# Optimization experiments

Measured on AMD Instinct MI355X. Metric: run time of the kernel, lower is better.

## Reference

```python
import jax, jax.numpy as jnp
import numpy as np

S = 2048      # words in the sentence
LMAX = 16     # max chars per word (padded)
VOCAB = 50000
ALPHA = 256
CE = 256      # char_embedding_dim (also char-LSTM hidden)
WE = 512      # word_embedding_dim
H = 1024      # hidden_dim of word LSTM


def setup_inputs() -> dict:
    key = jax.random.key(0)
    ks = jax.random.split(key, 13)
    def u(k, shape, scale):
        return jax.random.uniform(k, shape, jnp.float32, -scale, scale)
    sc_c = 1.0 / np.sqrt(CE).astype(np.float32)   # torch LSTM init scale
    sc_w = 1.0 / np.sqrt(H).astype(np.float32)
    return {
        "word_idxs": jax.random.randint(ks[0], (S,), 0, VOCAB),
        "char_idxs": jax.random.randint(ks[1], (S, LMAX), 0, ALPHA),
        "char_lens": jax.random.randint(ks[2], (S,), 1, LMAX + 1),
        "char_emb": jax.random.normal(ks[3], (ALPHA, CE), jnp.float32) * 0.1,
        "word_emb": jax.random.normal(ks[4], (VOCAB, WE), jnp.float32) * 0.1,
        "Wih_c": u(ks[5], (4 * CE, CE), sc_c),
        "Whh_c": u(ks[6], (4 * CE, CE), sc_c),
        "bih_c": u(ks[7], (4 * CE,), sc_c),
        "bhh_c": u(ks[8], (4 * CE,), sc_c),
        "Wih_w": u(ks[9], (4 * H, WE + CE), sc_w),
        "Whh_w": u(ks[10], (4 * H, H), sc_w),
        "bih_w": u(ks[11], (4 * H,), sc_w),
        "bhh_w": u(ks[12], (4 * H,), sc_w),
    }


def _lstm_scan(xs, Wih, Whh, bih, bhh, hdim):
    """Single-layer LSTM, torch gate order (i, f, g, o). xs: [T, B, D] -> hs [T, B, hdim]."""
    B = xs.shape[1]
    bias = bih + bhh
    def step(carry, x):
        h, c = carry
        gates = x @ Wih.T + h @ Whh.T + bias  # [B, 4*hdim]
        i, f, g, o = jnp.split(gates, 4, axis=-1)
        c = jax.nn.sigmoid(f) * c + jax.nn.sigmoid(i) * jnp.tanh(g)
        h = jax.nn.sigmoid(o) * jnp.tanh(c)
        return (h, c), h
    init = (jnp.zeros((B, hdim), xs.dtype), jnp.zeros((B, hdim), xs.dtype))
    _, hs = jax.lax.scan(step, init, xs)
    return hs


def reference(word_idxs, char_idxs, char_lens, char_emb, word_emb,
              Wih_c, Whh_c, bih_c, bhh_c, Wih_w, Whh_w, bih_w, bhh_w):
    # Char LSTM: batch all S words together (fuses the per-word Python loop).
    # Causality makes output at t = len-1 identical to running the true-length seq.
    ce = char_emb[char_idxs]                  # [S, LMAX, CE]
    ce = jnp.swapaxes(ce, 0, 1)               # [LMAX, S, CE] time-major
    hs = _lstm_scan(ce, Wih_c, Whh_c, bih_c, bhh_c, CE)   # [LMAX, S, CE]
    hs = jnp.swapaxes(hs, 0, 1)               # [S, LMAX, CE]
    last = jnp.take_along_axis(hs, (char_lens - 1)[:, None, None], axis=1)[:, 0]  # [S, CE]

    we = word_emb[word_idxs]                  # [S, WE]
    lstm_in = jnp.concatenate([we, last], axis=-1)[:, None, :]  # [S, 1, WE+CE]
    out = _lstm_scan(lstm_in, Wih_w, Whh_w, bih_w, bhh_w, H)    # [S, 1, H]
    # dropout p=0.0 -> identity
    return out
```

## Files before the change

### kernel.cpp

```cpp
#include <hip/hip_runtime.h>
#include <stdint.h>

#define S_WORDS 2048
#define LMAX    16
#define CE      256
#define WE      512
#define HDIM    1024
#define GC      1024
#define GW      4096
#define KW      768
#define NWG_RNN 128
#define NWB_WIN 512

#define IN_GATES_OFF 0
#define LAST_OFF     33554432
#define WT2C_OFF     35651584
#define WT2W_OFF     37748736
#define RING_OFF     WT2C_OFF
#define FLAGS_OFF    (RING_OFF + 3 * HDIM * 8)

typedef float f32x4 __attribute__((ext_vector_type(4)));

static __device__ __forceinline__ float sigm(float x) { return 1.0f / (1.0f + __expf(-x)); }
static __device__ __forceinline__ float tanh_fast(float x) {
    float ax = fminf(fabsf(x), 15.0f);
    float e  = __expf(2.0f * ax);
    float t  = (e - 1.0f) / (e + 1.0f);
    return copysignf(t, x);
}

__global__ void prep_c_kernel(const float* __restrict__ Wih,
                              const float* __restrict__ Whh,
                              float2* __restrict__ WT2c) {
    int idx = blockIdx.x * blockDim.x + threadIdx.x;
    if (idx >= 256 * GC) return;
    int kp = idx >> 10, row = idx & (GC - 1);
    int k = kp * 2;
    float2 v;
    if (k < CE) { v.x = Wih[row * CE + k];      v.y = Wih[row * CE + k + 1]; }
    else        { v.x = Whh[row * CE + k - CE]; v.y = Whh[row * CE + k - CE + 1]; }
    WT2c[idx] = v;
}

__global__ void prep_w_kernel(const float* __restrict__ Wih,
                              float2* __restrict__ WT2w) {
    int idx = blockIdx.x * blockDim.x + threadIdx.x;
    if (idx >= 384 * GW) return;
    int kp = idx >> 12, row = idx & (GW - 1);
    float2 v;
    v.x = Wih[row * KW + 2 * kp];
    v.y = Wih[row * KW + 2 * kp + 1];
    WT2w[idx] = v;
}

__global__ void __launch_bounds__(256) char_lstm_kernel(
    const int* __restrict__ char_idxs,
    const int* __restrict__ char_lens,
    const float* __restrict__ char_emb,
    const float* __restrict__ bih,
    const float* __restrict__ bhh,
    const float2* __restrict__ WT2c,
    float* __restrict__ last_out)
{
    __shared__ float xh[8][2 * CE];
    const int j = threadIdx.x;
    const int wbase = blockIdx.x * 8;

    float bias[4];
    #pragma unroll
    for (int g = 0; g < 4; g++) bias[g] = bih[g * CE + j] + bhh[g * CE + j];

    int len[8];
    float c[8];
    #pragma unroll
    for (int w = 0; w < 8; w++) {
        c[w] = 0.0f;
        xh[w][CE + j] = 0.0f;
        len[w] = char_lens[wbase + w];
    }

    for (int t = 0; t < LMAX; t++) {
        #pragma unroll
        for (int w = 0; w < 8; w++) {
            int ci = char_idxs[(wbase + w) * LMAX + t];
            xh[w][j] = char_emb[ci * CE + j];
        }
        __syncthreads();

        float acc[4][8];
        #pragma unroll
        for (int g = 0; g < 4; g++)
            #pragma unroll
            for (int w = 0; w < 8; w++) acc[g][w] = 0.0f;

        for (int kp = 0; kp < CE; kp++) {
            float2 wv[4];
            #pragma unroll
            for (int g = 0; g < 4; g++) wv[g] = WT2c[kp * GC + g * CE + j];
            #pragma unroll
            for (int w = 0; w < 8; w++) {
                float2 xv = *(const float2*)&xh[w][2 * kp];
                #pragma unroll
                for (int g = 0; g < 4; g++)
                    acc[g][w] = fmaf(wv[g].y, xv.y, fmaf(wv[g].x, xv.x, acc[g][w]));
            }
        }
        __syncthreads();

        #pragma unroll
        for (int w = 0; w < 8; w++) {
            float iv = sigm(acc[0][w] + bias[0]);
            float fv = sigm(acc[1][w] + bias[1]);
            float gv = tanhf(acc[2][w] + bias[2]);
            float ov = sigm(acc[3][w] + bias[3]);
            c[w] = fv * c[w] + iv * gv;
            float h = ov * tanhf(c[w]);
            xh[w][CE + j] = h;
            if (t == len[w] - 1) last_out[(wbase + w) * CE + j] = h;
        }
    }
}

__global__ void __launch_bounds__(512, 2) fused_word_kernel(
    const float* __restrict__ Whh,
    const int* __restrict__ word_idxs,
    const float* __restrict__ word_emb,
    const float* __restrict__ last,
    const float2* __restrict__ WT2w,
    const float* __restrict__ bih,
    const float* __restrict__ bhh,
    float* __restrict__ in_gates,
    unsigned long long* __restrict__ ring,
    unsigned int* __restrict__ flags,
    float* __restrict__ out)
{
    __shared__ float smem[8 * KW];
    const int tid = threadIdx.x;

    if (blockIdx.x >= NWG_RNN) {
        const int nb    = blockIdx.x - NWG_RNN;
        const int grp   = nb >> 1;
        const int half  = nb & 1;
        const int jj    = tid & 255;
        const int gh    = tid >> 8;
        const int rb2   = half * 2 + gh;
        const int wbase = grp * 8;
        float (*xh)[KW] = (float(*)[KW])smem;

        for (int w = 0; w < 8; w++) {
            int wi = word_idxs[wbase + w];
            xh[w][tid] = word_emb[(size_t)wi * WE + tid];
            if (tid < 256) xh[w][WE + tid] = last[(wbase + w) * CE + tid];
        }
        __syncthreads();

        float acc[4][8];
        #pragma unroll
        for (int g = 0; g < 4; g++)
            #pragma unroll
            for (int w = 0; w < 8; w++) acc[g][w] = 0.0f;

        for (int kp = 0; kp < KW / 2; kp++) {
            float2 wv[4];
            #pragma unroll
            for (int g = 0; g < 4; g++) wv[g] = WT2w[(size_t)kp * GW + rb2 * GC + g * CE + jj];
            #pragma unroll
            for (int w = 0; w < 8; w++) {
                float2 xv = *(const float2*)&xh[w][2 * kp];
                #pragma unroll
                for (int g = 0; g < 4; g++)
                    acc[g][w] = fmaf(wv[g].y, xv.y, fmaf(wv[g].x, xv.x, acc[g][w]));
            }
        }

        #pragma unroll
        for (int g = 0; g < 4; g++) {
            int row = rb2 * GC + g * CE + jj;
            float bias = bih[row] + bhh[row];
            #pragma unroll
            for (int w = 0; w < 8; w++)
                __hip_atomic_store(in_gates + (size_t)(wbase + w) * GW + row,
                                   acc[g][w] + bias,
                                   __ATOMIC_RELAXED, __HIP_MEMORY_SCOPE_AGENT);
        }
        __syncthreads();
        if (tid == 0)
            __hip_atomic_fetch_add(flags + grp, 1u,
                                   __ATOMIC_RELEASE, __HIP_MEMORY_SCOPE_AGENT);
        return;
    }

    const int v = tid >> 6;
    const int l = tid & 63;
    const int unit = blockIdx.x * 8 + v;
    float (*hbb)[HDIM] = (float(*)[HDIM])smem;

    f32x4 w[4][4];
    #pragma unroll
    for (int g = 0; g < 4; g++)
        #pragma unroll
        for (int cc = 0; cc < 4; cc++)
            w[g][cc] = *(const f32x4*)(Whh + (size_t)(g * HDIM + unit) * HDIM
                                       + cc * 256 + l * 4);
    #pragma unroll
    for (int g = 0; g < 4; g++)
        #pragma unroll
        for (int cc = 0; cc < 4; cc++)
            asm volatile("" : "+v"(w[g][cc]));

    float c_reg = 0.0f;

    for (int t = 0; t < S_WORDS; t++) {
        if ((t & 7) == 0) {
            const unsigned int* fl = flags + (t >> 3);
            while (__hip_atomic_load(fl, __ATOMIC_RELAXED, __HIP_MEMORY_SCOPE_AGENT) < 2u) {}
        }

        float ing0 = 0.f, ing1 = 0.f, ing2 = 0.f, ing3 = 0.f;
        if (l == 0) {
            const float* ig = in_gates + (size_t)t * GW + unit;
            ing0 = __hip_atomic_load(ig + 0 * HDIM, __ATOMIC_RELAXED, __HIP_MEMORY_SCOPE_AGENT);
            ing1 = __hip_atomic_load(ig + 1 * HDIM, __ATOMIC_RELAXED, __HIP_MEMORY_SCOPE_AGENT);
            ing2 = __hip_atomic_load(ig + 2 * HDIM, __ATOMIC_RELAXED, __HIP_MEMORY_SCOPE_AGENT);
            ing3 = __hip_atomic_load(ig + 3 * HDIM, __ATOMIC_RELAXED, __HIP_MEMORY_SCOPE_AGENT);
        }

        const unsigned long long* slot = ring + (size_t)(t % 3) * HDIM + v * 128;
        unsigned long long a0 = 0, a1 = 0;
        bool ok0 = false, ok1 = false;
        do {
            if (!ok0) {
                a0 = __hip_atomic_load(slot + l,      __ATOMIC_RELAXED, __HIP_MEMORY_SCOPE_AGENT);
                ok0 = ((unsigned)(a0 >> 32) == (unsigned)t);
            }
            if (!ok1) {
                a1 = __hip_atomic_load(slot + 64 + l, __ATOMIC_RELAXED, __HIP_MEMORY_SCOPE_AGENT);
                ok1 = ((unsigned)(a1 >> 32) == (unsigned)t);
            }
        } while (!__all(ok0 && ok1));
        {
            union { unsigned u32; float f; } c0, c1;
            c0.u32 = (unsigned)a0; c1.u32 = (unsigned)a1;
            hbb[t & 1][v * 128 + l]      = c0.f;
            hbb[t & 1][v * 128 + 64 + l] = c1.f;
        }
        __syncthreads();

        float acc0 = 0.f, acc1 = 0.f, acc2 = 0.f, acc3 = 0.f;
        const float* hb = hbb[t & 1];
        #pragma unroll
        for (int cc = 0; cc < 4; cc++) {
            f32x4 hv = *(const f32x4*)&hb[cc * 256 + l * 4];
            #pragma unroll
            for (int e = 0; e < 4; e++) {
                acc0 = fmaf(w[0][cc][e], hv[e], acc0);
                acc1 = fmaf(w[1][cc][e], hv[e], acc1);
                acc2 = fmaf(w[2][cc][e], hv[e], acc2);
                acc3 = fmaf(w[3][cc][e], hv[e], acc3);
            }
        }
        #pragma unroll
        for (int off = 32; off >= 1; off >>= 1) {
            acc0 += __shfl_xor(acc0, off, 64);
            acc1 += __shfl_xor(acc1, off, 64);
            acc2 += __shfl_xor(acc2, off, 64);
            acc3 += __shfl_xor(acc3, off, 64);
        }

        if (l == 0) {
            float iv = sigm(acc0 + ing0);
            float fv = sigm(acc1 + ing1);
            float gv = tanh_fast(acc2 + ing2);
            float ov = sigm(acc3 + ing3);
            c_reg = fv * c_reg + iv * gv;
            float h = ov * tanh_fast(c_reg);
            union { float f; unsigned u32; } cv; cv.f = h;
            unsigned long long pv =
                ((unsigned long long)(unsigned)(t + 1) << 32) | (unsigned long long)cv.u32;
            __hip_atomic_store(ring + (size_t)((t + 1) % 3) * HDIM + unit, pv,
                               __ATOMIC_RELAXED, __HIP_MEMORY_SCOPE_AGENT);
            out[(size_t)t * HDIM + unit] = h;
        }
    }
}

extern "C" void kernel_launch(void* const* d_in, const int* in_sizes, int n_in,
                              void* d_out, int out_size, void* d_ws, size_t ws_size,
                              hipStream_t stream) {
    const int* word_idxs = (const int*)d_in[0];
    const int* char_idxs = (const int*)d_in[1];
    const int* char_lens = (const int*)d_in[2];
    const float* char_emb = (const float*)d_in[3];
    const float* word_emb = (const float*)d_in[4];
    const float* Wih_c = (const float*)d_in[5];
    const float* Whh_c = (const float*)d_in[6];
    const float* bih_c = (const float*)d_in[7];
    const float* bhh_c = (const float*)d_in[8];
    const float* Wih_w = (const float*)d_in[9];
    const float* Whh_w = (const float*)d_in[10];
    const float* bih_w = (const float*)d_in[11];
    const float* bhh_w = (const float*)d_in[12];

    char* ws = (char*)d_ws;
    float*  in_gates = (float*)(ws + IN_GATES_OFF);
    float*  last     = (float*)(ws + LAST_OFF);
    float2* WT2c     = (float2*)(ws + WT2C_OFF);
    float2* WT2w     = (float2*)(ws + WT2W_OFF);
    unsigned long long* ring = (unsigned long long*)(ws + RING_OFF);
    unsigned int* flags      = (unsigned int*)(ws + FLAGS_OFF);

    hipLaunchKernelGGL(prep_c_kernel, dim3(1024), dim3(256), 0, stream,
                       Wih_c, Whh_c, WT2c);
    hipLaunchKernelGGL(prep_w_kernel, dim3(6144), dim3(256), 0, stream,
                       Wih_w, WT2w);
    hipLaunchKernelGGL(char_lstm_kernel, dim3(256), dim3(256), 0, stream,
                       char_idxs, char_lens, char_emb, bih_c, bhh_c, WT2c, last);
    hipMemsetAsync(ws + RING_OFF, 0,
                   3 * HDIM * sizeof(unsigned long long) + 256 * sizeof(unsigned int),
                   stream);
    hipLaunchKernelGGL(fused_word_kernel, dim3(NWG_RNN + NWB_WIN), dim3(512), 0, stream,
                       Whh_w, word_idxs, word_emb, last, WT2w, bih_w, bhh_w,
                       in_gates, ring, flags, (float*)d_out);
}
```

Before: 5.611 ms.

## Replace per-step workgroup barrier with per-wave LDS flags and chunked consumption

Removes the __syncthreads in the word-LSTM recurrence. Each wave publishes a workgroup-scope release flag once it has written its slice of h into LDS. Each wave then processes the four 256-element chunks in a staggered order, waiting only on the two waves that produced each chunk, so computation can start before every wave has arrived. The ring polling is double-buffered so two loads are in flight, and s_setprio raises wave priority during the critical compute phase. The risk is extra LDS flag traffic and spin overhead, and LDS size has to cover the flags.

```diff
diff --git a/kernel.cpp b/kernel.cpp
--- a/kernel.cpp
+++ b/kernel.cpp
@@ -20,6 +20,8 @@
 #define FLAGS_OFF    (RING_OFF + 3 * HDIM * 8)
 
 typedef float f32x4 __attribute__((ext_vector_type(4)));
+
+#define LD_AGENT(p) __hip_atomic_load((p), __ATOMIC_RELAXED, __HIP_MEMORY_SCOPE_AGENT)
 
 static __device__ __forceinline__ float sigm(float x) { return 1.0f / (1.0f + __expf(-x)); }
 static __device__ __forceinline__ float tanh_fast(float x) {
@@ -194,6 +196,9 @@
     const int l = tid & 63;
     const int unit = blockIdx.x * 8 + v;
     float (*hbb)[HDIM] = (float(*)[HDIM])smem;
+    unsigned int* hflag = (unsigned int*)(smem + 2 * HDIM);
+
+    if (tid < 8) hflag[tid] = 0u;
 
     f32x4 w[4][4];
     #pragma unroll
@@ -208,48 +213,77 @@
         for (int cc = 0; cc < 4; cc++)
             asm volatile("" : "+v"(w[g][cc]));
 
+    __syncthreads();
+
     float c_reg = 0.0f;
 
     for (int t = 0; t < S_WORDS; t++) {
         if ((t & 7) == 0) {
             const unsigned int* fl = flags + (t >> 3);
-            while (__hip_atomic_load(fl, __ATOMIC_RELAXED, __HIP_MEMORY_SCOPE_AGENT) < 2u) {}
+            while (LD_AGENT(fl) < 2u) {}
         }
 
         float ing0 = 0.f, ing1 = 0.f, ing2 = 0.f, ing3 = 0.f;
         if (l == 0) {
             const float* ig = in_gates + (size_t)t * GW + unit;
-            ing0 = __hip_atomic_load(ig + 0 * HDIM, __ATOMIC_RELAXED, __HIP_MEMORY_SCOPE_AGENT);
-            ing1 = __hip_atomic_load(ig + 1 * HDIM, __ATOMIC_RELAXED, __HIP_MEMORY_SCOPE_AGENT);
-            ing2 = __hip_atomic_load(ig + 2 * HDIM, __ATOMIC_RELAXED, __HIP_MEMORY_SCOPE_AGENT);
-            ing3 = __hip_atomic_load(ig + 3 * HDIM, __ATOMIC_RELAXED, __HIP_MEMORY_SCOPE_AGENT);
-        }
-
-        const unsigned long long* slot = ring + (size_t)(t % 3) * HDIM + v * 128;
-        unsigned long long a0 = 0, a1 = 0;
+            ing0 = LD_AGENT(ig + 0 * HDIM);
+            ing1 = LD_AGENT(ig + 1 * HDIM);
+            ing2 = LD_AGENT(ig + 2 * HDIM);
+            ing3 = LD_AGENT(ig + 3 * HDIM);
+        }
+
+        const unsigned long long* sA = ring + (size_t)(t % 3) * HDIM + v * 128 + l;
+        const unsigned long long* sB = sA + 64;
+        unsigned long long p0 = LD_AGENT(sA), p1 = LD_AGENT(sB);
+        unsigned long long q0 = LD_AGENT(sA), q1 = LD_AGENT(sB);
         bool ok0 = false, ok1 = false;
-        do {
-            if (!ok0) {
-                a0 = __hip_atomic_load(slot + l,      __ATOMIC_RELAXED, __HIP_MEMORY_SCOPE_AGENT);
-                ok0 = ((unsigned)(a0 >> 32) == (unsigned)t);
-            }
-            if (!ok1) {
-                a1 = __hip_atomic_load(slot + 64 + l, __ATOMIC_RELAXED, __HIP_MEMORY_SCOPE_AGENT);
-                ok1 = ((unsigned)(a1 >> 32) == (unsigned)t);
-            }
-        } while (!__all(ok0 && ok1));
+        unsigned long long h0 = 0, h1 = 0;
+        const unsigned tt = (unsigned)t;
+        for (;;) {
+            if (!ok0 && (unsigned)(p0 >> 32) == tt) { h0 = p0; ok0 = true; }
+            if (!ok1 && (unsigned)(p1 >> 32) == tt) { h1 = p1; ok1 = true; }
+            if (__all(ok0 && ok1)) break;
+            if (!ok0) p0 = LD_AGENT(sA);
+            if (!ok1) p1 = LD_AGENT(sB);
+            if (!ok0 && (unsigned)(q0 >> 32) == tt) { h0 = q0; ok0 = true; }
+            if (!ok1 && (unsigned)(q1 >> 32) == tt) { h1 = q1; ok1 = true; }
+            if (__all(ok0 && ok1)) break;
+            if (!ok0) q0 = LD_AGENT(sA);
+            if (!ok1) q1 = LD_AGENT(sB);
+        }
+
+        __builtin_amdgcn_s_setprio(1);
+
+        float* hb = hbb[t & 1];
         {
-            union { unsigned u32; float f; } c0, c1;
-            c0.u32 = (unsigned)a0; c1.u32 = (unsigned)a1;
-            hbb[t & 1][v * 128 + l]      = c0.f;
-            hbb[t & 1][v * 128 + 64 + l] = c1.f;
-        }
-        __syncthreads();
+            union { unsigned u; float f; } c0, c1;
+            c0.u = (unsigned)h0; c1.u = (unsigned)h1;
+            hb[v * 128 + l]      = c0.f;
+            hb[v * 128 + 64 + l] = c1.f;
+        }
+        if (l == 0)
+            __hip_atomic_store(&hflag[v], (unsigned)(t + 1),
+                               __ATOMIC_RELEASE, __HIP_MEMORY_SCOPE_WORKGROUP);
 
         float acc0 = 0.f, acc1 = 0.f, acc2 = 0.f, acc3 = 0.f;
-        const float* hb = hbb[t & 1];
-        #pragma unroll
-        for (int cc = 0; cc < 4; cc++) {
+        const unsigned tgt = (unsigned)(t + 1);
+        #pragma unroll
+        for (int q = 0; q < 4; q++) {
+            const int cc = ((v >> 1) + q) & 3;
+            if (__hip_atomic_load(&hflag[2 * cc], __ATOMIC_ACQUIRE,
+                                  __HIP_MEMORY_SCOPE_WORKGROUP) < tgt) {
+                __builtin_amdgcn_s_setprio(0);
+                while (__hip_atomic_load(&hflag[2 * cc], __ATOMIC_ACQUIRE,
+                                         __HIP_MEMORY_SCOPE_WORKGROUP) < tgt) {}
+                __builtin_amdgcn_s_setprio(1);
+            }
+            if (__hip_atomic_load(&hflag[2 * cc + 1], __ATOMIC_ACQUIRE,
+                                  __HIP_MEMORY_SCOPE_WORKGROUP) < tgt) {
+                __builtin_amdgcn_s_setprio(0);
+                while (__hip_atomic_load(&hflag[2 * cc + 1], __ATOMIC_ACQUIRE,
+                                         __HIP_MEMORY_SCOPE_WORKGROUP) < tgt) {}
+                __builtin_amdgcn_s_setprio(1);
+            }
             f32x4 hv = *(const f32x4*)&hb[cc * 256 + l * 4];
             #pragma unroll
             for (int e = 0; e < 4; e++) {
@@ -259,6 +293,7 @@
                 acc3 = fmaf(w[3][cc][e], hv[e], acc3);
             }
         }
+
         #pragma unroll
         for (int off = 32; off >= 1; off >>= 1) {
             acc0 += __shfl_xor(acc0, off, 64);
@@ -281,6 +316,7 @@
                                __ATOMIC_RELAXED, __HIP_MEMORY_SCOPE_AGENT);
             out[(size_t)t * HDIM + unit] = h;
         }
+        __builtin_amdgcn_s_setprio(0);
     }
 }
 
```

Result: slower. 15.21 ms (+171.1%).
